# Kernel tuning notes

Hardware: AMD Instinct MI355X
Metric: run time of the kernel (lower is better)

## Reference

```python
import jax, jax.numpy as jnp
import numpy as np

EPS = 1e-5
NH = 4          # num_heads
DH = 128        # head_dim
ALPHA = 1.0 / float(np.sqrt(DH))


def _ln(x, w, b):
    m = x.mean(-1, keepdims=True)
    v = x.var(-1, keepdims=True)
    return (x - m) * jax.lax.rsqrt(v + EPS) * w + b


def setup_inputs() -> dict:
    key = jax.random.key(0)
    ks = jax.random.split(key, 8)
    D = 512                 # hidden_size
    U = 4 * NH * DH         # uvqk linear out = 2048
    B, S, H = 32, 256, 2048  # batch, new tokens/seq, history len/seq
    NT = B * S              # 8192 flattened jagged tokens
    layer_input = jax.random.normal(ks[0], (NT, D), dtype=jnp.float32)
    hist_k = jax.random.normal(ks[1], (B, H, NH, DH), dtype=jnp.float32) * 0.1
    hist_v = jax.random.normal(ks[2], (B, H, NH, DH), dtype=jnp.float32) * 0.1
    # torch init: uniform(-0.5, 0.5); scaled down for numerical sanity
    W_uvqk = (jax.random.uniform(ks[3], (D, U), dtype=jnp.float32) - 0.5) * 0.1
    b_uvqk = (jax.random.uniform(ks[4], (U,), dtype=jnp.float32) - 0.5) * 0.1
    ln_in_w = jnp.ones((D,), jnp.float32)
    ln_in_b = jnp.zeros((D,), jnp.float32)
    ln_out_w = jnp.ones((NH * DH,), jnp.float32)
    ln_out_b = jnp.zeros((NH * DH,), jnp.float32)
    W_proj = jax.random.normal(ks[5], (NH * DH, D), dtype=jnp.float32) * 0.05
    return {
        "layer_input": layer_input, "hist_k": hist_k, "hist_v": hist_v,
        "ln_in_w": ln_in_w, "ln_in_b": ln_in_b,
        "W_uvqk": W_uvqk, "b_uvqk": b_uvqk,
        "ln_out_w": ln_out_w, "ln_out_b": ln_out_b, "W_proj": W_proj,
    }


def reference(layer_input, hist_k, hist_v, ln_in_w, ln_in_b,
              W_uvqk, b_uvqk, ln_out_w, ln_out_b, W_proj):
    B, H, nh, dh = hist_k.shape
    NT, D = layer_input.shape
    S = NT // B
    dspl = nh * dh
    # ln -> linear+bias -> silu (fused u,v,q,k projection)
    x = _ln(layer_input, ln_in_w, ln_in_b)
    uvqk = jax.nn.silu(x @ W_uvqk + b_uvqk)
    u, v, q, k = jnp.split(uvqk, 4, axis=-1)   # order: user, value, query, key
    q = q.reshape(B, S, nh, dh)
    k = k.reshape(B, S, nh, dh)
    v = v.reshape(B, S, nh, dh)
    # paged KV-cache append == concat new k,v after history
    K = jnp.concatenate([hist_k, k], axis=1)   # [B, T, nh, dh], T = H+S
    V = jnp.concatenate([hist_v, v], axis=1)
    T = H + S
    # HSTU varlen attention: silu(alpha * q k^T) with causal delta-q mask,
    # query i sits at global position H+i and may attend to kv pos <= H+i
    scores = jnp.einsum('bsnd,btnd->bnst', q, K) * ALPHA
    mask = jnp.arange(T)[None, :] <= (H + jnp.arange(S))[:, None]  # [S, T]
    p = jnp.where(mask[None, None], jax.nn.silu(scores), 0.0)
    attn = jnp.einsum('bnst,btnd->bsnd', p, V).reshape(NT, dspl)
    # gated output LN, projection, residual
    parallel = u * _ln(attn, ln_out_w, ln_out_b)
    return parallel @ W_proj + layer_input
```

## Files before the change

kernel.cpp:

```cpp
#include <hip/hip_runtime.h>
#include <hip/hip_bf16.h>


typedef __attribute__((ext_vector_type(8))) short v8s;
typedef __attribute__((ext_vector_type(4))) float v4f;
typedef __attribute__((ext_vector_type(16))) float v16f;
typedef __attribute__((ext_vector_type(4))) unsigned short v4us;
typedef __attribute__((ext_vector_type(4))) unsigned int v4u;

#define D_HID 512
#define U_DIM 2048
#define NHEAD 4
#define DHEAD 128
#define BATCH 32
#define SEQ   256
#define HIST  2048
#define NTOK  8192
#define ALPHA_ 0.08838834764831845f
#define EPS_   1e-5f

__device__ __forceinline__ unsigned short f2bf(float f) {
  unsigned int u = __float_as_uint(f);
  u += 0x7FFFu + ((u >> 16) & 1u);
  return (unsigned short)(u >> 16);
}
__device__ __forceinline__ float bf2f(unsigned short s) {
  return __uint_as_float(((unsigned int)s) << 16);
}
__device__ __forceinline__ float siluf(float x) {
  return x * __builtin_amdgcn_rcpf(1.0f + __expf(-x));
}
__device__ __forceinline__ unsigned int cvtpk(float lo, float hi) {
  __hip_bfloat162 h = __float22bfloat162_rn(make_float2(lo, hi));
  union { __hip_bfloat162 h; unsigned int u; } cv; cv.h = h;
  return cv.u;
}

__global__ __launch_bounds__(256) void ln_in_kernel(
    const float* __restrict__ x, const float* __restrict__ w,
    const float* __restrict__ b, unsigned short* __restrict__ out)
{
  int wid = threadIdx.x >> 6, lane = threadIdx.x & 63;
  int row = blockIdx.x * 4 + wid;
  const float* xr = x + (size_t)row * D_HID + lane * 8;
  float4 a0 = *(const float4*)xr;
  float4 a1 = *(const float4*)(xr + 4);
  float v[8] = {a0.x, a0.y, a0.z, a0.w, a1.x, a1.y, a1.z, a1.w};
  float s = 0.f, s2 = 0.f;
#pragma unroll
  for (int j = 0; j < 8; ++j) { s += v[j]; s2 += v[j] * v[j]; }
#pragma unroll
  for (int m = 1; m < 64; m <<= 1) { s += __shfl_xor(s, m, 64); s2 += __shfl_xor(s2, m, 64); }
  float mean = s * (1.f / D_HID);
  float var  = s2 * (1.f / D_HID) - mean * mean;
  float rstd = rsqrtf(var + EPS_);
  const float* wp = w + lane * 8; const float* bp = b + lane * 8;
  float4 w0 = *(const float4*)wp, w1 = *(const float4*)(wp + 4);
  float4 b0 = *(const float4*)bp, b1 = *(const float4*)(bp + 4);
  float wv[8] = {w0.x, w0.y, w0.z, w0.w, w1.x, w1.y, w1.z, w1.w};
  float bv[8] = {b0.x, b0.y, b0.z, b0.w, b1.x, b1.y, b1.z, b1.w};
  v8s o;
#pragma unroll
  for (int j = 0; j < 8; ++j) o[j] = (short)f2bf((v[j] - mean) * rstd * wv[j] + bv[j]);
  *(v8s*)(out + (size_t)row * D_HID + lane * 8) = o;
}

__global__ __launch_bounds__(256) void gated_ln_kernel(
    const float* __restrict__ attn0, const float* __restrict__ attn1,
    const unsigned short* __restrict__ uvqk,
    const float* __restrict__ w, const float* __restrict__ b,
    unsigned short* __restrict__ par)
{
  int wid = threadIdx.x >> 6, lane = threadIdx.x & 63;
  int row = blockIdx.x * 4 + wid;
  size_t off = (size_t)row * D_HID + lane * 8;
  float4 x0 = *(const float4*)(attn0 + off), x1 = *(const float4*)(attn0 + off + 4);
  float4 y0 = *(const float4*)(attn1 + off), y1 = *(const float4*)(attn1 + off + 4);
  float v[8] = {x0.x + y0.x, x0.y + y0.y, x0.z + y0.z, x0.w + y0.w,
                x1.x + y1.x, x1.y + y1.y, x1.z + y1.z, x1.w + y1.w};
  float s = 0.f, s2 = 0.f;
#pragma unroll
  for (int j = 0; j < 8; ++j) { s += v[j]; s2 += v[j] * v[j]; }
#pragma unroll
  for (int m = 1; m < 64; m <<= 1) { s += __shfl_xor(s, m, 64); s2 += __shfl_xor(s2, m, 64); }
  float mean = s * (1.f / D_HID);
  float var  = s2 * (1.f / D_HID) - mean * mean;
  float rstd = rsqrtf(var + EPS_);
  const float* wp = w + lane * 8; const float* bp = b + lane * 8;
  float4 w0 = *(const float4*)wp, w1 = *(const float4*)(wp + 4);
  float4 b0 = *(const float4*)bp, b1 = *(const float4*)(bp + 4);
  float wv[8] = {w0.x, w0.y, w0.z, w0.w, w1.x, w1.y, w1.z, w1.w};
  float bv[8] = {b0.x, b0.y, b0.z, b0.w, b1.x, b1.y, b1.z, b1.w};
  v8s uv = *(const v8s*)(uvqk + (size_t)row * U_DIM + lane * 8);
  v8s o;
#pragma unroll
  for (int j = 0; j < 8; ++j) {
    float u = bf2f((unsigned short)uv[j]);
    o[j] = (short)f2bf(u * ((v[j] - mean) * rstd * wv[j] + bv[j]));
  }
  *(v8s*)(par + (size_t)row * D_HID + lane * 8) = o;
}

__global__ __launch_bounds__(256) void transpose_w_kernel(
    const float* __restrict__ in, unsigned short* __restrict__ out, int R, int C)
{
  __shared__ float tile[32][33];
  int c0 = blockIdx.x * 32, r0 = blockIdx.y * 32;
  int tr = threadIdx.x >> 3;
  int tc = (threadIdx.x & 7) * 4;
  float4 vv = *(const float4*)(in + (size_t)(r0 + tr) * C + c0 + tc);
  tile[tr][tc + 0] = vv.x; tile[tr][tc + 1] = vv.y;
  tile[tr][tc + 2] = vv.z; tile[tr][tc + 3] = vv.w;
  __syncthreads();
  v4us o;
#pragma unroll
  for (int j = 0; j < 4; ++j) o[j] = f2bf(tile[tc + j][tr]);
  *(v4us*)(out + (size_t)(c0 + tr) * R + r0 + tc) = o;
}

template <int EPI>
__global__ __launch_bounds__(256) void gemm_kernel(
    const unsigned short* __restrict__ A, const unsigned short* __restrict__ Bt,
    int K, int N,
    const float* __restrict__ bias, const float* __restrict__ resid,
    unsigned short* __restrict__ outb, float* __restrict__ outf)
{
  __shared__ unsigned short Al[128 * 40];
  __shared__ unsigned short Bl[128 * 40];
  int m0 = blockIdx.x * 128, n0 = blockIdx.y * 128;
  int tid = threadIdx.x, lane = tid & 63, wid = tid >> 6;
  int wr = wid >> 1, wc = wid & 1;
  int lr = lane & 15, lg = lane >> 4;

  v4f acc[4][4];
#pragma unroll
  for (int i = 0; i < 4; ++i)
#pragma unroll
    for (int j = 0; j < 4; ++j) acc[i][j] = (v4f){0.f, 0.f, 0.f, 0.f};

  int srow = tid >> 1;
  int sc   = (tid & 1) * 16;
  const unsigned short* ga = A  + (size_t)(m0 + srow) * K + sc;
  const unsigned short* gb = Bt + (size_t)(n0 + srow) * K + sc;

  for (int k0 = 0; k0 < K; k0 += 32) {
    v8s a0 = *(const v8s*)(ga + k0);
    v8s a1 = *(const v8s*)(ga + k0 + 8);
    v8s b0 = *(const v8s*)(gb + k0);
    v8s b1 = *(const v8s*)(gb + k0 + 8);
    *(v8s*)&Al[srow * 40 + sc]     = a0;
    *(v8s*)&Al[srow * 40 + sc + 8] = a1;
    *(v8s*)&Bl[srow * 40 + sc]     = b0;
    *(v8s*)&Bl[srow * 40 + sc + 8] = b1;
    __syncthreads();
    v8s af[4], bf[4];
#pragma unroll
    for (int mt = 0; mt < 4; ++mt) af[mt] = *(const v8s*)&Al[(wr * 64 + mt * 16 + lr) * 40 + lg * 8];
#pragma unroll
    for (int nt = 0; nt < 4; ++nt) bf[nt] = *(const v8s*)&Bl[(wc * 64 + nt * 16 + lr) * 40 + lg * 8];
#pragma unroll
    for (int mt = 0; mt < 4; ++mt)
#pragma unroll
      for (int nt = 0; nt < 4; ++nt)
        acc[mt][nt] = __builtin_amdgcn_mfma_f32_16x16x32_bf16(af[mt], bf[nt], acc[mt][nt], 0, 0, 0);
    __syncthreads();
  }

#pragma unroll
  for (int nt = 0; nt < 4; ++nt) {
    int col = n0 + wc * 64 + nt * 16 + lr;
    float bi = 0.f;
    if constexpr (EPI == 0) bi = bias[col];
#pragma unroll
    for (int mt = 0; mt < 4; ++mt) {
      int row0 = m0 + wr * 64 + mt * 16 + lg * 4;
#pragma unroll
      for (int r = 0; r < 4; ++r) {
        float xv = acc[mt][nt][r];
        if constexpr (EPI == 0) {
          float rv = siluf(xv + bi);
          if ((unsigned)(col - 2 * D_HID) < (unsigned)D_HID) rv *= ALPHA_;
          outb[(size_t)(row0 + r) * N + col] = f2bf(rv);
        } else {
          outf[(size_t)(row0 + r) * N + col] = xv + resid[(size_t)(row0 + r) * N + col];
        }
      }
    }
  }
}

__global__ __launch_bounds__(512, 2) void attn_kernel(
    const float* __restrict__ histK, const float* __restrict__ histV,
    const unsigned short* __restrict__ uvqk, float* __restrict__ attn_out)
{
  __shared__ __align__(16) unsigned short Kl[2 * 64 * 128];
  __shared__ __align__(16) unsigned short Vt[2 * 128 * 64];

  int bid = blockIdx.x;
  int q   = bid >> 7;
  int b   = (bid >> 2) & 31;
  int n   = bid & 3;
  int tbase0 = q * 1152;
  const int NT = 18;

  int tid = threadIdx.x, lane = tid & 63, w = tid >> 6;
  int l5 = lane & 31;
  int hi = lane >> 5;
  int hi8 = hi * 8;
  int sq = w * 32 + l5;

  v8s qf[8];
  {
    const unsigned short* qp = uvqk + (size_t)(b * SEQ + sq) * U_DIM
                               + 2 * D_HID + n * DHEAD + hi8;
#pragma unroll
    for (int ks = 0; ks < 8; ++ks) qf[ks] = *(const v8s*)(qp + ks * 16);
  }

  v16f oacc[4];
#pragma unroll
  for (int i = 0; i < 4; ++i)
#pragma unroll
    for (int r = 0; r < 16; ++r) oacc[i][r] = 0.f;

  int m     = tid & 15;
  int std0  = m * 8;
  int strow = tid >> 4;

  const float* kbase = histK + (((size_t)b * HIST) * NHEAD + n) * DHEAD + std0;
  const float* vbase = histV + (((size_t)b * HIST) * NHEAD + n) * DHEAD + std0;
  const unsigned short* nkbase = uvqk + (size_t)(b * SEQ) * U_DIM + 3 * D_HID + n * DHEAD + std0;
  const unsigned short* nvbase = uvqk + (size_t)(b * SEQ) * U_DIM + 1 * D_HID + n * DHEAD + std0;

  float4 hx[2][4];
  v8s    nx[2][2];
  int isnew_r = 0;

  auto stage_load = [&](int kt) {
    int tb = tbase0 + kt * 64;
    if (tb < HIST) {
      isnew_r = 0;
#pragma unroll
      for (int p = 0; p < 2; ++p) {
        unsigned off = ((unsigned)(tb + 2 * strow + p)) << 9;
        hx[p][0] = *(const float4*)(kbase + off);
        hx[p][1] = *(const float4*)(kbase + off + 4);
        hx[p][2] = *(const float4*)(vbase + off);
        hx[p][3] = *(const float4*)(vbase + off + 4);
      }
    } else {
      isnew_r = 1;
#pragma unroll
      for (int p = 0; p < 2; ++p) {
        unsigned off = ((unsigned)(tb - HIST + 2 * strow + p)) << 11;
        nx[p][0] = *(const v8s*)(nkbase + off);
        nx[p][1] = *(const v8s*)(nvbase + off);
      }
    }
  };

  auto stage_store = [&](int buf) {
    unsigned short* Kb = &Kl[buf * 8192];
    unsigned short* Vb = &Vt[buf * 8192];
    int t0 = 2 * strow;
    if (!isnew_r) {
#pragma unroll
      for (int p = 0; p < 2; ++p) {
        int t = t0 + p;
        v4u kp;
        kp[0] = cvtpk(hx[p][0].x, hx[p][0].y);
        kp[1] = cvtpk(hx[p][0].z, hx[p][0].w);
        kp[2] = cvtpk(hx[p][1].x, hx[p][1].y);
        kp[3] = cvtpk(hx[p][1].z, hx[p][1].w);
        *(v4u*)&Kb[t * 128 + (std0 ^ ((t & 7) << 3))] = kp;
      }
      float v0[8] = {hx[0][2].x, hx[0][2].y, hx[0][2].z, hx[0][2].w,
                     hx[0][3].x, hx[0][3].y, hx[0][3].z, hx[0][3].w};
      float v1[8] = {hx[1][2].x, hx[1][2].y, hx[1][2].z, hx[1][2].w,
                     hx[1][3].x, hx[1][3].y, hx[1][3].z, hx[1][3].w};
#pragma unroll
      for (int j = 0; j < 8; ++j) {
        int d = std0 + j;
        int col = t0 ^ ((((d >> 3) ^ d) & 7) << 3);
        *(unsigned int*)&Vb[d * 64 + col] = cvtpk(v0[j], v1[j]);
      }
    } else {
#pragma unroll
      for (int p = 0; p < 2; ++p) {
        int t = t0 + p;
        *(v8s*)&Kb[t * 128 + (std0 ^ ((t & 7) << 3))] = nx[p][0];
      }
#pragma unroll
      for (int j = 0; j < 8; ++j) {
        int d = std0 + j;
        int col = t0 ^ ((((d >> 3) ^ d) & 7) << 3);
        unsigned int pk = (unsigned int)(unsigned short)nx[0][1][j]
                        | ((unsigned int)(unsigned short)nx[1][1][j] << 16);
        *(unsigned int*)&Vb[d * 64 + col] = pk;
      }
    }
  };

  stage_load(0);
  stage_store(0);
  stage_load(1);
  __syncthreads();

  for (int kt = 0; kt < NT; ++kt) {
    int cur = kt & 1;
    if (kt + 1 < NT) stage_store(cur ^ 1);
    if (kt + 2 < NT) stage_load(kt + 2);

    int tb = tbase0 + kt * 64;
    bool masked = (tb >= HIST);
    const unsigned short* Kb = &Kl[cur * 8192];
    const unsigned short* Vb = &Vt[cur * 8192];

    __builtin_amdgcn_s_setprio(1);

    v8s pb[4];
#pragma unroll
    for (int tt = 0; tt < 2; ++tt) {
      v16f sa;
#pragma unroll
      for (int r = 0; r < 16; ++r) sa[r] = 0.f;
      int trow = tt * 32 + l5;
      int kx = (trow & 7) << 3;
      int krow = trow * 128;
#pragma unroll
      for (int ks = 0; ks < 8; ++ks) {
        v8s kf = *(const v8s*)&Kb[krow + ((ks * 16 + hi8) ^ kx)];
        sa = __builtin_amdgcn_mfma_f32_32x32x16_bf16(kf, qf[ks], sa, 0, 0, 0);
      }
      unsigned e[8];
      if (masked) {
        int thr = sq - (tb - HIST) - tt * 32 - 4 * hi;
#pragma unroll
        for (int i = 0; i < 8; ++i) {
          int r0 = 2 * i, r1 = 2 * i + 1;
          int tl0 = (r0 & 3) + 8 * (r0 >> 2);
          int tl1 = (r1 & 3) + 8 * (r1 >> 2);
          float p0 = (tl0 <= thr) ? siluf(sa[r0]) : 0.f;
          float p1 = (tl1 <= thr) ? siluf(sa[r1]) : 0.f;
          e[i] = cvtpk(p0, p1);
        }
      } else {
#pragma unroll
        for (int i = 0; i < 8; ++i) e[i] = cvtpk(siluf(sa[2 * i]), siluf(sa[2 * i + 1]));
      }
#pragma unroll
      for (int h = 0; h < 2; ++h) {
        unsigned a0 = e[h * 4 + 0], a1 = e[h * 4 + 1];
        unsigned b0 = e[h * 4 + 2], b1 = e[h * 4 + 3];
        unsigned sa0 = (unsigned)__shfl_xor((int)a0, 32, 64);
        unsigned sa1 = (unsigned)__shfl_xor((int)a1, 32, 64);
        unsigned sb0 = (unsigned)__shfl_xor((int)b0, 32, 64);
        unsigned sb1 = (unsigned)__shfl_xor((int)b1, 32, 64);
        union { unsigned u[4]; v8s s; } U;
        U.u[0] = hi ? sb0 : a0;
        U.u[1] = hi ? sb1 : a1;
        U.u[2] = hi ? b0 : sa0;
        U.u[3] = hi ? b1 : sa1;
        pb[tt * 2 + h] = U.s;
      }
    }

#pragma unroll
    for (int ks = 0; ks < 4; ++ks) {
#pragma unroll
      for (int dt4 = 0; dt4 < 4; ++dt4) {
        int d = dt4 * 32 + l5;
        int col = (ks * 16 + hi8) ^ ((((d >> 3) ^ d) & 7) << 3);
        v8s vf = *(const v8s*)&Vb[d * 64 + col];
        oacc[dt4] = __builtin_amdgcn_mfma_f32_32x32x16_bf16(vf, pb[ks], oacc[dt4], 0, 0, 0);
      }
    }
    __builtin_amdgcn_s_setprio(0);

    if (kt + 1 < NT) __syncthreads();
  }

  {
    float* op = attn_out + (size_t)q * ((size_t)NTOK * D_HID)
              + (size_t)(b * SEQ + sq) * D_HID + n * DHEAD + 4 * hi;
#pragma unroll
    for (int dt4 = 0; dt4 < 4; ++dt4) {
#pragma unroll
      for (int g = 0; g < 4; ++g) {
        float4 o4 = make_float4(oacc[dt4][4 * g + 0], oacc[dt4][4 * g + 1],
                                oacc[dt4][4 * g + 2], oacc[dt4][4 * g + 3]);
        *(float4*)(op + dt4 * 32 + 8 * g) = o4;
      }
    }
  }
}

extern "C" void kernel_launch(void* const* d_in, const int* in_sizes, int n_in,
                              void* d_out, int out_size, void* d_ws, size_t ws_size,
                              hipStream_t stream)
{
  (void)in_sizes; (void)n_in; (void)out_size; (void)ws_size;

  const float* layer_input = (const float*)d_in[0];
  const float* hist_k   = (const float*)d_in[1];
  const float* hist_v   = (const float*)d_in[2];
  const float* ln_in_w  = (const float*)d_in[3];
  const float* ln_in_b  = (const float*)d_in[4];
  const float* W_uvqk   = (const float*)d_in[5];
  const float* b_uvqk   = (const float*)d_in[6];
  const float* ln_out_w = (const float*)d_in[7];
  const float* ln_out_b = (const float*)d_in[8];
  const float* W_proj   = (const float*)d_in[9];
  float* out = (float*)d_out;

  char* ws = (char*)d_ws;
  unsigned short* uvqk    = (unsigned short*)(ws);
  float*          attn0   = (float*)         (ws + (32u << 20));
  float*          attn1   = (float*)         (ws + (48u << 20));
  unsigned short* x_bf    = (unsigned short*)(ws + (48u << 20));
  unsigned short* par     = (unsigned short*)(ws + (64u << 20));
  unsigned short* wt_uvqk = (unsigned short*)(ws + (72u << 20));
  unsigned short* wt_proj = (unsigned short*)(ws + (74u << 20));

  ln_in_kernel<<<dim3(2048), dim3(256), 0, stream>>>(layer_input, ln_in_w, ln_in_b, x_bf);
  transpose_w_kernel<<<dim3(64, 16), dim3(256), 0, stream>>>(W_uvqk, wt_uvqk, 512, 2048);
  transpose_w_kernel<<<dim3(16, 16), dim3(256), 0, stream>>>(W_proj, wt_proj, 512, 512);
  gemm_kernel<0><<<dim3(64, 16), dim3(256), 0, stream>>>(x_bf, wt_uvqk, 512, 2048,
                                                         b_uvqk, nullptr, uvqk, nullptr);
  attn_kernel<<<dim3(256), dim3(512), 0, stream>>>(hist_k, hist_v, uvqk, attn0);
  gated_ln_kernel<<<dim3(2048), dim3(256), 0, stream>>>(attn0, attn1, uvqk, ln_out_w, ln_out_b, par);
  gemm_kernel<1><<<dim3(64, 4), dim3(256), 0, stream>>>(par, wt_proj, 512, 512,
                                                        nullptr, layer_input, nullptr, out);
}
```

Before: 170.3 us.

## Split attention KV into four chunks with 256-thread blocks handling two query sets

```diff
diff --git a/kernel.cpp b/kernel.cpp
--- a/kernel.cpp
+++ b/kernel.cpp
@@ -67,6 +67,7 @@
 
 __global__ __launch_bounds__(256) void gated_ln_kernel(
     const float* __restrict__ attn0, const float* __restrict__ attn1,
+    const float* __restrict__ attn2, const float* __restrict__ attn3,
     const unsigned short* __restrict__ uvqk,
     const float* __restrict__ w, const float* __restrict__ b,
     unsigned short* __restrict__ par)
@@ -76,8 +77,12 @@
   size_t off = (size_t)row * D_HID + lane * 8;
   float4 x0 = *(const float4*)(attn0 + off), x1 = *(const float4*)(attn0 + off + 4);
   float4 y0 = *(const float4*)(attn1 + off), y1 = *(const float4*)(attn1 + off + 4);
-  float v[8] = {x0.x + y0.x, x0.y + y0.y, x0.z + y0.z, x0.w + y0.w,
-                x1.x + y1.x, x1.y + y1.y, x1.z + y1.z, x1.w + y1.w};
+  float4 z0 = *(const float4*)(attn2 + off), z1 = *(const float4*)(attn2 + off + 4);
+  float4 u0 = *(const float4*)(attn3 + off), u1 = *(const float4*)(attn3 + off + 4);
+  float v[8] = {x0.x + y0.x + z0.x + u0.x, x0.y + y0.y + z0.y + u0.y,
+                x0.z + y0.z + z0.z + u0.z, x0.w + y0.w + z0.w + u0.w,
+                x1.x + y1.x + z1.x + u1.x, x1.y + y1.y + z1.y + u1.y,
+                x1.z + y1.z + z1.z + u1.z, x1.w + y1.w + z1.w + u1.w};
   float s = 0.f, s2 = 0.f;
 #pragma unroll
   for (int j = 0; j < 8; ++j) { s += v[j]; s2 += v[j] * v[j]; }
@@ -189,7 +194,7 @@
   }
 }
 
-__global__ __launch_bounds__(512, 2) void attn_kernel(
+__global__ __launch_bounds__(256, 2) void attn_kernel(
     const float* __restrict__ histK, const float* __restrict__ histV,
     const unsigned short* __restrict__ uvqk, float* __restrict__ attn_out)
 {
@@ -200,49 +205,50 @@
   int q   = bid >> 7;
   int b   = (bid >> 2) & 31;
   int n   = bid & 3;
-  int tbase0 = q * 1152;
-  const int NT = 18;
+  int tbase0 = q * 576;
+  const int NT = 9;
 
   int tid = threadIdx.x, lane = tid & 63, w = tid >> 6;
   int l5 = lane & 31;
   int hi = lane >> 5;
   int hi8 = hi * 8;
-  int sq = w * 32 + l5;
-
-  v8s qf[8];
-  {
-    const unsigned short* qp = uvqk + (size_t)(b * SEQ + sq) * U_DIM
+
+  v8s qf[2][8];
+#pragma unroll
+  for (int set = 0; set < 2; ++set) {
+    const unsigned short* qp = uvqk + (size_t)(b * SEQ + w * 64 + set * 32 + l5) * U_DIM
                                + 2 * D_HID + n * DHEAD + hi8;
 #pragma unroll
-    for (int ks = 0; ks < 8; ++ks) qf[ks] = *(const v8s*)(qp + ks * 16);
-  }
-
-  v16f oacc[4];
-#pragma unroll
-  for (int i = 0; i < 4; ++i)
-#pragma unroll
-    for (int r = 0; r < 16; ++r) oacc[i][r] = 0.f;
+    for (int ks = 0; ks < 8; ++ks) qf[set][ks] = *(const v8s*)(qp + ks * 16);
+  }
+
+  v16f oacc[2][4];
+#pragma unroll
+  for (int set = 0; set < 2; ++set)
+#pragma unroll
+    for (int i = 0; i < 4; ++i)
+#pragma unroll
+      for (int r = 0; r < 16; ++r) oacc[set][i][r] = 0.f;
 
   int m     = tid & 15;
   int std0  = m * 8;
   int strow = tid >> 4;
 
-  const float* kbase = histK + (((size_t)b * HIST) * NHEAD + n) * DHEAD + std0;
-  const float* vbase = histV + (((size_t)b * HIST) * NHEAD + n) * DHEAD + std0;
-  const unsigned short* nkbase = uvqk + (size_t)(b * SEQ) * U_DIM + 3 * D_HID + n * DHEAD + std0;
-  const unsigned short* nvbase = uvqk + (size_t)(b * SEQ) * U_DIM + 1 * D_HID + n * DHEAD + std0;
+  const float* kbase = histK + (((size_t)b * HIST) * NHEAD + n) * DHEAD;
+  const float* vbase = histV + (((size_t)b * HIST) * NHEAD + n) * DHEAD;
+  const unsigned short* nkbase = uvqk + (size_t)(b * SEQ) * U_DIM + 3 * D_HID + n * DHEAD;
+  const unsigned short* nvbase = uvqk + (size_t)(b * SEQ) * U_DIM + 1 * D_HID + n * DHEAD;
 
   float4 hx[2][4];
-  v8s    nx[2][2];
   int isnew_r = 0;
 
-  auto stage_load = [&](int kt) {
-    int tb = tbase0 + kt * 64;
+  auto stage_load = [&](int kt, int h) {
+    int tb = tbase0 + kt * 64 + h * 32;
     if (tb < HIST) {
       isnew_r = 0;
 #pragma unroll
       for (int p = 0; p < 2; ++p) {
-        unsigned off = ((unsigned)(tb + 2 * strow + p)) << 9;
+        unsigned off = (((unsigned)(tb + 2 * strow + p)) << 9) + std0;
         hx[p][0] = *(const float4*)(kbase + off);
         hx[p][1] = *(const float4*)(kbase + off + 4);
         hx[p][2] = *(const float4*)(vbase + off);
@@ -252,17 +258,17 @@
       isnew_r = 1;
 #pragma unroll
       for (int p = 0; p < 2; ++p) {
-        unsigned off = ((unsigned)(tb - HIST + 2 * strow + p)) << 11;
-        nx[p][0] = *(const v8s*)(nkbase + off);
-        nx[p][1] = *(const v8s*)(nvbase + off);
+        unsigned off = (((unsigned)(tb - HIST + 2 * strow + p)) << 11) + std0;
+        hx[p][0] = *(const float4*)(nkbase + off);
+        hx[p][2] = *(const float4*)(nvbase + off);
       }
     }
   };
 
-  auto stage_store = [&](int buf) {
+  auto stage_store = [&](int buf, int h) {
     unsigned short* Kb = &Kl[buf * 8192];
     unsigned short* Vb = &Vt[buf * 8192];
-    int t0 = 2 * strow;
+    int t0 = h * 32 + 2 * strow;
     if (!isnew_r) {
 #pragma unroll
       for (int p = 0; p < 2; ++p) {
@@ -285,31 +291,33 @@
         *(unsigned int*)&Vb[d * 64 + col] = cvtpk(v0[j], v1[j]);
       }
     } else {
+      union { float4 f; v8s s; } ck0, ck1, cv0, cv1;
+      ck0.f = hx[0][0]; ck1.f = hx[1][0];
+      cv0.f = hx[0][2]; cv1.f = hx[1][2];
 #pragma unroll
       for (int p = 0; p < 2; ++p) {
         int t = t0 + p;
-        *(v8s*)&Kb[t * 128 + (std0 ^ ((t & 7) << 3))] = nx[p][0];
+        *(v8s*)&Kb[t * 128 + (std0 ^ ((t & 7) << 3))] = p ? ck1.s : ck0.s;
       }
 #pragma unroll
       for (int j = 0; j < 8; ++j) {
         int d = std0 + j;
         int col = t0 ^ ((((d >> 3) ^ d) & 7) << 3);
-        unsigned int pk = (unsigned int)(unsigned short)nx[0][1][j]
-                        | ((unsigned int)(unsigned short)nx[1][1][j] << 16);
+        unsigned int pk = (unsigned int)(unsigned short)cv0.s[j]
+                        | ((unsigned int)(unsigned short)cv1.s[j] << 16);
         *(unsigned int*)&Vb[d * 64 + col] = pk;
       }
     }
   };
 
-  stage_load(0);
-  stage_store(0);
-  stage_load(1);
+  stage_load(0, 0); stage_store(0, 0);
+  stage_load(0, 1); stage_store(0, 1);
+  stage_load(1, 0);
   __syncthreads();
 
   for (int kt = 0; kt < NT; ++kt) {
     int cur = kt & 1;
-    if (kt + 1 < NT) stage_store(cur ^ 1);
-    if (kt + 2 < NT) stage_load(kt + 2);
+    if (kt + 1 < NT) { stage_store(cur ^ 1, 0); stage_load(kt + 1, 1); }
 
     int tb = tbase0 + kt * 64;
     bool masked = (tb >= HIST);
@@ -317,54 +325,63 @@
     const unsigned short* Vb = &Vt[cur * 8192];
 
     __builtin_amdgcn_s_setprio(1);
-
-    v8s pb[4];
+    v8s pb[2][4];
 #pragma unroll
     for (int tt = 0; tt < 2; ++tt) {
-      v16f sa;
-#pragma unroll
-      for (int r = 0; r < 16; ++r) sa[r] = 0.f;
       int trow = tt * 32 + l5;
       int kx = (trow & 7) << 3;
-      int krow = trow * 128;
+      const unsigned short* kr = Kb + trow * 128;
+      v16f sacc[2];
+#pragma unroll
+      for (int r = 0; r < 16; ++r) { sacc[0][r] = 0.f; sacc[1][r] = 0.f; }
 #pragma unroll
       for (int ks = 0; ks < 8; ++ks) {
-        v8s kf = *(const v8s*)&Kb[krow + ((ks * 16 + hi8) ^ kx)];
-        sa = __builtin_amdgcn_mfma_f32_32x32x16_bf16(kf, qf[ks], sa, 0, 0, 0);
-      }
-      unsigned e[8];
-      if (masked) {
-        int thr = sq - (tb - HIST) - tt * 32 - 4 * hi;
-#pragma unroll
-        for (int i = 0; i < 8; ++i) {
-          int r0 = 2 * i, r1 = 2 * i + 1;
-          int tl0 = (r0 & 3) + 8 * (r0 >> 2);
-          int tl1 = (r1 & 3) + 8 * (r1 >> 2);
-          float p0 = (tl0 <= thr) ? siluf(sa[r0]) : 0.f;
-          float p1 = (tl1 <= thr) ? siluf(sa[r1]) : 0.f;
-          e[i] = cvtpk(p0, p1);
+        v8s kf = *(const v8s*)&kr[(ks * 16 + hi8) ^ kx];
+        sacc[0] = __builtin_amdgcn_mfma_f32_32x32x16_bf16(kf, qf[0][ks], sacc[0], 0, 0, 0);
+        sacc[1] = __builtin_amdgcn_mfma_f32_32x32x16_bf16(kf, qf[1][ks], sacc[1], 0, 0, 0);
+      }
+#pragma unroll
+      for (int set = 0; set < 2; ++set) {
+        unsigned e[8];
+        if (masked) {
+          int thr = (w * 64 + set * 32 + l5) - (tb - HIST) - tt * 32 - 4 * hi;
+#pragma unroll
+          for (int i = 0; i < 8; ++i) {
+            int r0 = 2 * i, r1 = r0 + 1;
+            int tl0 = (r0 & 3) + 8 * (r0 >> 2);
+            int tl1 = (r1 & 3) + 8 * (r1 >> 2);
+            float p0 = (tl0 <= thr) ? siluf(sacc[set][r0]) : 0.f;
+            float p1 = (tl1 <= thr) ? siluf(sacc[set][r1]) : 0.f;
+            e[i] = cvtpk(p0, p1);
+          }
+        } else {
+#pragma unroll
+          for (int i = 0; i < 8; ++i)
+            e[i] = cvtpk(siluf(sacc[set][2 * i]), siluf(sacc[set][2 * i + 1]));
         }
-      } else {
-#pragma unroll
-        for (int i = 0; i < 8; ++i) e[i] = cvtpk(siluf(sa[2 * i]), siluf(sa[2 * i + 1]));
-      }
-#pragma unroll
-      for (int h = 0; h < 2; ++h) {
-        unsigned a0 = e[h * 4 + 0], a1 = e[h * 4 + 1];
-        unsigned b0 = e[h * 4 + 2], b1 = e[h * 4 + 3];
-        unsigned sa0 = (unsigned)__shfl_xor((int)a0, 32, 64);
-        unsigned sa1 = (unsigned)__shfl_xor((int)a1, 32, 64);
-        unsigned sb0 = (unsigned)__shfl_xor((int)b0, 32, 64);
-        unsigned sb1 = (unsigned)__shfl_xor((int)b1, 32, 64);
-        union { unsigned u[4]; v8s s; } U;
-        U.u[0] = hi ? sb0 : a0;
-        U.u[1] = hi ? sb1 : a1;
-        U.u[2] = hi ? b0 : sa0;
-        U.u[3] = hi ? b1 : sa1;
-        pb[tt * 2 + h] = U.s;
-      }
-    }
-
+#pragma unroll
+        for (int h = 0; h < 2; ++h) {
+          unsigned a0 = e[h * 4 + 0], a1 = e[h * 4 + 1];
+          unsigned b0 = e[h * 4 + 2], b1 = e[h * 4 + 3];
+          unsigned x0 = (unsigned)__shfl_xor((int)a0, 32, 64);
+          unsigned x1 = (unsigned)__shfl_xor((int)a1, 32, 64);
+          unsigned x2 = (unsigned)__shfl_xor((int)b0, 32, 64);
+          unsigned x3 = (unsigned)__shfl_xor((int)b1, 32, 64);
+          union { unsigned u[4]; v8s s; } U;
+          U.u[0] = hi ? x2 : a0;
+          U.u[1] = hi ? x3 : a1;
+          U.u[2] = hi ? b0 : x0;
+          U.u[3] = hi ? b1 : x1;
+          pb[set][tt * 2 + h] = U.s;
+        }
+      }
+    }
+    __builtin_amdgcn_s_setprio(0);
+
+    if (kt + 1 < NT) stage_store(cur ^ 1, 1);
+    if (kt + 2 < NT) stage_load(kt + 2, 0);
+
+    __builtin_amdgcn_s_setprio(1);
 #pragma unroll
     for (int ks = 0; ks < 4; ++ks) {
 #pragma unroll
@@ -372,7 +389,8 @@
         int d = dt4 * 32 + l5;
         int col = (ks * 16 + hi8) ^ ((((d >> 3) ^ d) & 7) << 3);
         v8s vf = *(const v8s*)&Vb[d * 64 + col];
-        oacc[dt4] = __builtin_amdgcn_mfma_f32_32x32x16_bf16(vf, pb[ks], oacc[dt4], 0, 0, 0);
+        oacc[0][dt4] = __builtin_amdgcn_mfma_f32_32x32x16_bf16(vf, pb[0][ks], oacc[0][dt4], 0, 0, 0);
+        oacc[1][dt4] = __builtin_amdgcn_mfma_f32_32x32x16_bf16(vf, pb[1][ks], oacc[1][dt4], 0, 0, 0);
       }
     }
     __builtin_amdgcn_s_setprio(0);
@@ -380,15 +398,17 @@
     if (kt + 1 < NT) __syncthreads();
   }
 
-  {
+#pragma unroll
+  for (int set = 0; set < 2; ++set) {
     float* op = attn_out + (size_t)q * ((size_t)NTOK * D_HID)
-              + (size_t)(b * SEQ + sq) * D_HID + n * DHEAD + 4 * hi;
+              + (size_t)(b * SEQ + w * 64 + set * 32 + l5) * D_HID
+              + n * DHEAD + 4 * hi;
 #pragma unroll
     for (int dt4 = 0; dt4 < 4; ++dt4) {
 #pragma unroll
       for (int g = 0; g < 4; ++g) {
-        float4 o4 = make_float4(oacc[dt4][4 * g + 0], oacc[dt4][4 * g + 1],
-                                oacc[dt4][4 * g + 2], oacc[dt4][4 * g + 3]);
+        float4 o4 = make_float4(oacc[set][dt4][4 * g + 0], oacc[set][dt4][4 * g + 1],
+                                oacc[set][dt4][4 * g + 2], oacc[set][dt4][4 * g + 3]);
         *(float4*)(op + dt4 * 32 + 8 * g) = o4;
       }
     }
@@ -415,20 +435,23 @@
 
   char* ws = (char*)d_ws;
   unsigned short* uvqk    = (unsigned short*)(ws);
-  float*          attn0   = (float*)         (ws + (32u << 20));
-  float*          attn1   = (float*)         (ws + (48u << 20));
-  unsigned short* x_bf    = (unsigned short*)(ws + (48u << 20));
-  unsigned short* par     = (unsigned short*)(ws + (64u << 20));
-  unsigned short* wt_uvqk = (unsigned short*)(ws + (72u << 20));
-  unsigned short* wt_proj = (unsigned short*)(ws + (74u << 20));
+  float*          attn0   = (float*)         (ws + (32u  << 20));
+  float*          attn1   = (float*)         (ws + (48u  << 20));
+  float*          attn2   = (float*)         (ws + (64u  << 20));
+  float*          attn3   = (float*)         (ws + (80u  << 20));
+  unsigned short* x_bf    = (unsigned short*)(ws + (96u  << 20));
+  unsigned short* par     = (unsigned short*)(ws + (96u  << 20));
+  unsigned short* wt_uvqk = (unsigned short*)(ws + (104u << 20));
+  unsigned short* wt_proj = (unsigned short*)(ws + (106u << 20));
 
   ln_in_kernel<<<dim3(2048), dim3(256), 0, stream>>>(layer_input, ln_in_w, ln_in_b, x_bf);
   transpose_w_kernel<<<dim3(64, 16), dim3(256), 0, stream>>>(W_uvqk, wt_uvqk, 512, 2048);
   transpose_w_kernel<<<dim3(16, 16), dim3(256), 0, stream>>>(W_proj, wt_proj, 512, 512);
   gemm_kernel<0><<<dim3(64, 16), dim3(256), 0, stream>>>(x_bf, wt_uvqk, 512, 2048,
                                                          b_uvqk, nullptr, uvqk, nullptr);
-  attn_kernel<<<dim3(256), dim3(512), 0, stream>>>(hist_k, hist_v, uvqk, attn0);
-  gated_ln_kernel<<<dim3(2048), dim3(256), 0, stream>>>(attn0, attn1, uvqk, ln_out_w, ln_out_b, par);
+  attn_kernel<<<dim3(512), dim3(256), 0, stream>>>(hist_k, hist_v, uvqk, attn0);
+  gated_ln_kernel<<<dim3(2048), dim3(256), 0, stream>>>(attn0, attn1, attn2, attn3,
+                                                        uvqk, ln_out_w, ln_out_b, par);
   gemm_kernel<1><<<dim3(64, 4), dim3(256), 0, stream>>>(par, wt_proj, 512, 512,
                                                         nullptr, layer_input, nullptr, out);
 }
```

After: 387.0 us. +127.2%, slower.

## Split attention blocks by query half and exchange P tiles across waves via LDS

Applied to the files above, without the earlier changes.

```diff
diff --git a/kernel.cpp b/kernel.cpp
--- a/kernel.cpp
+++ b/kernel.cpp
@@ -189,25 +189,32 @@
   }
 }
 
-__global__ __launch_bounds__(512, 2) void attn_kernel(
+__global__ __launch_bounds__(512, 4) void attn_kernel(
     const float* __restrict__ histK, const float* __restrict__ histV,
     const unsigned short* __restrict__ uvqk, float* __restrict__ attn_out)
 {
   __shared__ __align__(16) unsigned short Kl[2 * 64 * 128];
   __shared__ __align__(16) unsigned short Vt[2 * 128 * 64];
+  __shared__ unsigned int Pex[8][8][64];
 
   int bid = blockIdx.x;
-  int q   = bid >> 7;
+  int th  = bid >> 8;
+  int qb  = (bid >> 7) & 1;
   int b   = (bid >> 2) & 31;
   int n   = bid & 3;
-  int tbase0 = q * 1152;
-  const int NT = 18;
+  int tbase0 = th * 1152;
+  int NT = 18;
+  {
+    int nt2 = (HIST + qb * 128 + 127 - tbase0) / 64 + 1;
+    if (nt2 < NT) NT = nt2;
+  }
 
   int tid = threadIdx.x, lane = tid & 63, w = tid >> 6;
+  int g  = w & 3;
+  int h  = w >> 2;
   int l5 = lane & 31;
-  int hi = lane >> 5;
-  int hi8 = hi * 8;
-  int sq = w * 32 + l5;
+  int hi = lane >> 5, hi8 = hi * 8;
+  int sq = qb * 128 + g * 32 + l5;
 
   v8s qf[8];
   {
@@ -217,9 +224,9 @@
     for (int ks = 0; ks < 8; ++ks) qf[ks] = *(const v8s*)(qp + ks * 16);
   }
 
-  v16f oacc[4];
-#pragma unroll
-  for (int i = 0; i < 4; ++i)
+  v16f oacc[2];
+#pragma unroll
+  for (int i = 0; i < 2; ++i)
 #pragma unroll
     for (int r = 0; r < 16; ++r) oacc[i][r] = 0.f;
 
@@ -233,7 +240,6 @@
   const unsigned short* nvbase = uvqk + (size_t)(b * SEQ) * U_DIM + 1 * D_HID + n * DHEAD + std0;
 
   float4 hx[2][4];
-  v8s    nx[2][2];
   int isnew_r = 0;
 
   auto stage_load = [&](int kt) {
@@ -253,8 +259,8 @@
 #pragma unroll
       for (int p = 0; p < 2; ++p) {
         unsigned off = ((unsigned)(tb - HIST + 2 * strow + p)) << 11;
-        nx[p][0] = *(const v8s*)(nkbase + off);
-        nx[p][1] = *(const v8s*)(nvbase + off);
+        hx[p][0] = *(const float4*)(const void*)(nkbase + off);
+        hx[p][2] = *(const float4*)(const void*)(nvbase + off);
       }
     }
   };
@@ -285,17 +291,20 @@
         *(unsigned int*)&Vb[d * 64 + col] = cvtpk(v0[j], v1[j]);
       }
     } else {
+      union { float4 f; v8s s; } ck0, ck1, cv0, cv1;
+      ck0.f = hx[0][0]; ck1.f = hx[1][0];
+      cv0.f = hx[0][2]; cv1.f = hx[1][2];
 #pragma unroll
       for (int p = 0; p < 2; ++p) {
         int t = t0 + p;
-        *(v8s*)&Kb[t * 128 + (std0 ^ ((t & 7) << 3))] = nx[p][0];
+        *(v8s*)&Kb[t * 128 + (std0 ^ ((t & 7) << 3))] = p ? ck1.s : ck0.s;
       }
 #pragma unroll
       for (int j = 0; j < 8; ++j) {
         int d = std0 + j;
         int col = t0 ^ ((((d >> 3) ^ d) & 7) << 3);
-        unsigned int pk = (unsigned int)(unsigned short)nx[0][1][j]
-                        | ((unsigned int)(unsigned short)nx[1][1][j] << 16);
+        unsigned int pk = (unsigned int)(unsigned short)cv0.s[j]
+                        | ((unsigned int)(unsigned short)cv1.s[j] << 16);
         *(unsigned int*)&Vb[d * 64 + col] = pk;
       }
     }
@@ -316,15 +325,14 @@
     const unsigned short* Kb = &Kl[cur * 8192];
     const unsigned short* Vb = &Vt[cur * 8192];
 
+    v8s pb[4];
+
     __builtin_amdgcn_s_setprio(1);
-
-    v8s pb[4];
-#pragma unroll
-    for (int tt = 0; tt < 2; ++tt) {
+    {
       v16f sa;
 #pragma unroll
       for (int r = 0; r < 16; ++r) sa[r] = 0.f;
-      int trow = tt * 32 + l5;
+      int trow = h * 32 + l5;
       int kx = (trow & 7) << 3;
       int krow = trow * 128;
 #pragma unroll
@@ -334,7 +342,7 @@
       }
       unsigned e[8];
       if (masked) {
-        int thr = sq - (tb - HIST) - tt * 32 - 4 * hi;
+        int thr = sq - (tb - HIST) - h * 32 - 4 * hi;
 #pragma unroll
         for (int i = 0; i < 8; ++i) {
           int r0 = 2 * i, r1 = 2 * i + 1;
@@ -349,9 +357,9 @@
         for (int i = 0; i < 8; ++i) e[i] = cvtpk(siluf(sa[2 * i]), siluf(sa[2 * i + 1]));
       }
 #pragma unroll
-      for (int h = 0; h < 2; ++h) {
-        unsigned a0 = e[h * 4 + 0], a1 = e[h * 4 + 1];
-        unsigned b0 = e[h * 4 + 2], b1 = e[h * 4 + 3];
+      for (int hh = 0; hh < 2; ++hh) {
+        unsigned a0 = e[hh * 4 + 0], a1 = e[hh * 4 + 1];
+        unsigned b0 = e[hh * 4 + 2], b1 = e[hh * 4 + 3];
         unsigned sa0 = (unsigned)__shfl_xor((int)a0, 32, 64);
         unsigned sa1 = (unsigned)__shfl_xor((int)a1, 32, 64);
         unsigned sb0 = (unsigned)__shfl_xor((int)b0, 32, 64);
@@ -361,15 +369,39 @@
         U.u[1] = hi ? sb1 : a1;
         U.u[2] = hi ? b0 : sa0;
         U.u[3] = hi ? b1 : sa1;
-        pb[tt * 2 + h] = U.s;
-      }
-    }
-
+        pb[2 * h + hh] = U.s;
+      }
+    }
+    __builtin_amdgcn_s_setprio(0);
+
+    {
+      union { v8s s; unsigned u[4]; } F0, F1;
+      F0.s = pb[2 * h]; F1.s = pb[2 * h + 1];
+#pragma unroll
+      for (int j = 0; j < 4; ++j) {
+        Pex[w][j][lane]     = F0.u[j];
+        Pex[w][j + 4][lane] = F1.u[j];
+      }
+    }
+    __syncthreads();
+    {
+      int hp = 1 - h;
+      union { unsigned u[4]; v8s s; } G0, G1;
+#pragma unroll
+      for (int j = 0; j < 4; ++j) {
+        G0.u[j] = Pex[w ^ 4][j][lane];
+        G1.u[j] = Pex[w ^ 4][j + 4][lane];
+      }
+      pb[2 * hp]     = G0.s;
+      pb[2 * hp + 1] = G1.s;
+    }
+
+    __builtin_amdgcn_s_setprio(1);
 #pragma unroll
     for (int ks = 0; ks < 4; ++ks) {
 #pragma unroll
-      for (int dt4 = 0; dt4 < 4; ++dt4) {
-        int d = dt4 * 32 + l5;
+      for (int dt4 = 0; dt4 < 2; ++dt4) {
+        int d = h * 64 + dt4 * 32 + l5;
         int col = (ks * 16 + hi8) ^ ((((d >> 3) ^ d) & 7) << 3);
         v8s vf = *(const v8s*)&Vb[d * 64 + col];
         oacc[dt4] = __builtin_amdgcn_mfma_f32_32x32x16_bf16(vf, pb[ks], oacc[dt4], 0, 0, 0);
@@ -381,15 +413,15 @@
   }
 
   {
-    float* op = attn_out + (size_t)q * ((size_t)NTOK * D_HID)
-              + (size_t)(b * SEQ + sq) * D_HID + n * DHEAD + 4 * hi;
-#pragma unroll
-    for (int dt4 = 0; dt4 < 4; ++dt4) {
-#pragma unroll
-      for (int g = 0; g < 4; ++g) {
-        float4 o4 = make_float4(oacc[dt4][4 * g + 0], oacc[dt4][4 * g + 1],
-                                oacc[dt4][4 * g + 2], oacc[dt4][4 * g + 3]);
-        *(float4*)(op + dt4 * 32 + 8 * g) = o4;
+    float* op = attn_out + (size_t)th * ((size_t)NTOK * D_HID)
+              + (size_t)(b * SEQ + sq) * D_HID + n * DHEAD + h * 64 + 4 * hi;
+#pragma unroll
+    for (int dt4 = 0; dt4 < 2; ++dt4) {
+#pragma unroll
+      for (int gq = 0; gq < 4; ++gq) {
+        float4 o4 = make_float4(oacc[dt4][4 * gq + 0], oacc[dt4][4 * gq + 1],
+                                oacc[dt4][4 * gq + 2], oacc[dt4][4 * gq + 3]);
+        *(float4*)(op + dt4 * 32 + 8 * gq) = o4;
       }
     }
   }
@@ -427,7 +459,7 @@
   transpose_w_kernel<<<dim3(16, 16), dim3(256), 0, stream>>>(W_proj, wt_proj, 512, 512);
   gemm_kernel<0><<<dim3(64, 16), dim3(256), 0, stream>>>(x_bf, wt_uvqk, 512, 2048,
                                                          b_uvqk, nullptr, uvqk, nullptr);
-  attn_kernel<<<dim3(256), dim3(512), 0, stream>>>(hist_k, hist_v, uvqk, attn0);
+  attn_kernel<<<dim3(512), dim3(512), 0, stream>>>(hist_k, hist_v, uvqk, attn0);
   gated_ln_kernel<<<dim3(2048), dim3(256), 0, stream>>>(attn0, attn1, uvqk, ln_out_w, ln_out_b, par);
   gemm_kernel<1><<<dim3(64, 4), dim3(256), 0, stream>>>(par, wt_proj, 512, 512,
                                                         nullptr, layer_input, nullptr, out);
```

New measurement: 511.9 us. 3.01x slower.

## Use direct global-to-LDS loads with swizzle in GEMM and interleave QK MFMA chains

Applied to the files above, without the earlier changes.

```diff
diff --git a/kernel.cpp b/kernel.cpp
--- a/kernel.cpp
+++ b/kernel.cpp
@@ -125,12 +125,13 @@
     const float* __restrict__ bias, const float* __restrict__ resid,
     unsigned short* __restrict__ outb, float* __restrict__ outf)
 {
-  __shared__ unsigned short Al[128 * 40];
-  __shared__ unsigned short Bl[128 * 40];
+  __shared__ unsigned short Al[128 * 64];
+  __shared__ unsigned short Bl[128 * 64];
   int m0 = blockIdx.x * 128, n0 = blockIdx.y * 128;
   int tid = threadIdx.x, lane = tid & 63, wid = tid >> 6;
   int wr = wid >> 1, wc = wid & 1;
   int lr = lane & 15, lg = lane >> 4;
+  int rkey = (lr & 7) << 3;
 
   v4f acc[4][4];
 #pragma unroll
@@ -138,31 +139,38 @@
 #pragma unroll
     for (int j = 0; j < 4; ++j) acc[i][j] = (v4f){0.f, 0.f, 0.f, 0.f};
 
-  int srow = tid >> 1;
-  int sc   = (tid & 1) * 16;
-  const unsigned short* ga = A  + (size_t)(m0 + srow) * K + sc;
-  const unsigned short* gb = Bt + (size_t)(n0 + srow) * K + sc;
-
-  for (int k0 = 0; k0 < K; k0 += 32) {
-    v8s a0 = *(const v8s*)(ga + k0);
-    v8s a1 = *(const v8s*)(ga + k0 + 8);
-    v8s b0 = *(const v8s*)(gb + k0);
-    v8s b1 = *(const v8s*)(gb + k0 + 8);
-    *(v8s*)&Al[srow * 40 + sc]     = a0;
-    *(v8s*)&Al[srow * 40 + sc + 8] = a1;
-    *(v8s*)&Bl[srow * 40 + sc]     = b0;
-    *(v8s*)&Bl[srow * 40 + sc + 8] = b1;
+  int srow = tid >> 3;
+  int scol = ((tid & 7) * 8) ^ ((srow & 7) << 3);
+  const unsigned short* gA = A  + (size_t)(m0 + srow) * K + scol;
+  const unsigned short* gB = Bt + (size_t)(n0 + srow) * K + scol;
+
+  for (int k0 = 0; k0 < K; k0 += 64) {
+#pragma unroll
+    for (int c = 0; c < 4; ++c) {
+      __builtin_amdgcn_global_load_lds(
+          (const __attribute__((address_space(1))) unsigned int*)(gA + (size_t)(c * 32) * K + k0),
+          (__attribute__((address_space(3))) unsigned int*)&Al[c * 2048 + wid * 512], 16, 0, 0);
+      __builtin_amdgcn_global_load_lds(
+          (const __attribute__((address_space(1))) unsigned int*)(gB + (size_t)(c * 32) * K + k0),
+          (__attribute__((address_space(3))) unsigned int*)&Bl[c * 2048 + wid * 512], 16, 0, 0);
+    }
+    asm volatile("s_waitcnt vmcnt(0)" ::: "memory");
     __syncthreads();
-    v8s af[4], bf[4];
-#pragma unroll
-    for (int mt = 0; mt < 4; ++mt) af[mt] = *(const v8s*)&Al[(wr * 64 + mt * 16 + lr) * 40 + lg * 8];
-#pragma unroll
-    for (int nt = 0; nt < 4; ++nt) bf[nt] = *(const v8s*)&Bl[(wc * 64 + nt * 16 + lr) * 40 + lg * 8];
-#pragma unroll
-    for (int mt = 0; mt < 4; ++mt)
+#pragma unroll
+    for (int kk = 0; kk < 2; ++kk) {
+      v8s af[4], bf[4];
+#pragma unroll
+      for (int mt = 0; mt < 4; ++mt)
+        af[mt] = *(const v8s*)&Al[(wr * 64 + mt * 16 + lr) * 64 + ((kk * 32 + lg * 8) ^ rkey)];
 #pragma unroll
       for (int nt = 0; nt < 4; ++nt)
-        acc[mt][nt] = __builtin_amdgcn_mfma_f32_16x16x32_bf16(af[mt], bf[nt], acc[mt][nt], 0, 0, 0);
+        bf[nt] = *(const v8s*)&Bl[(wc * 64 + nt * 16 + lr) * 64 + ((kk * 32 + lg * 8) ^ rkey)];
+#pragma unroll
+      for (int mt = 0; mt < 4; ++mt)
+#pragma unroll
+        for (int nt = 0; nt < 4; ++nt)
+          acc[mt][nt] = __builtin_amdgcn_mfma_f32_16x16x32_bf16(af[mt], bf[nt], acc[mt][nt], 0, 0, 0);
+    }
     __syncthreads();
   }
 
@@ -319,49 +327,54 @@
     __builtin_amdgcn_s_setprio(1);
 
     v8s pb[4];
-#pragma unroll
-    for (int tt = 0; tt < 2; ++tt) {
-      v16f sa;
-#pragma unroll
-      for (int r = 0; r < 16; ++r) sa[r] = 0.f;
-      int trow = tt * 32 + l5;
-      int kx = (trow & 7) << 3;
-      int krow = trow * 128;
+    {
+      v16f sa0, sa1;
+#pragma unroll
+      for (int r = 0; r < 16; ++r) { sa0[r] = 0.f; sa1[r] = 0.f; }
+      int kx = (l5 & 7) << 3;
+      int krow = l5 * 128;
 #pragma unroll
       for (int ks = 0; ks < 8; ++ks) {
-        v8s kf = *(const v8s*)&Kb[krow + ((ks * 16 + hi8) ^ kx)];
-        sa = __builtin_amdgcn_mfma_f32_32x32x16_bf16(kf, qf[ks], sa, 0, 0, 0);
-      }
-      unsigned e[8];
-      if (masked) {
-        int thr = sq - (tb - HIST) - tt * 32 - 4 * hi;
-#pragma unroll
-        for (int i = 0; i < 8; ++i) {
-          int r0 = 2 * i, r1 = 2 * i + 1;
-          int tl0 = (r0 & 3) + 8 * (r0 >> 2);
-          int tl1 = (r1 & 3) + 8 * (r1 >> 2);
-          float p0 = (tl0 <= thr) ? siluf(sa[r0]) : 0.f;
-          float p1 = (tl1 <= thr) ? siluf(sa[r1]) : 0.f;
-          e[i] = cvtpk(p0, p1);
+        int off = (ks * 16 + hi8) ^ kx;
+        v8s kf0 = *(const v8s*)&Kb[krow + off];
+        v8s kf1 = *(const v8s*)&Kb[krow + 4096 + off];
+        sa0 = __builtin_amdgcn_mfma_f32_32x32x16_bf16(kf0, qf[ks], sa0, 0, 0, 0);
+        sa1 = __builtin_amdgcn_mfma_f32_32x32x16_bf16(kf1, qf[ks], sa1, 0, 0, 0);
+      }
+#pragma unroll
+      for (int tt = 0; tt < 2; ++tt) {
+        v16f sa = tt ? sa1 : sa0;
+        unsigned e[8];
+        if (masked) {
+          int thr = sq - (tb - HIST) - tt * 32 - 4 * hi;
+#pragma unroll
+          for (int i = 0; i < 8; ++i) {
+            int r0 = 2 * i, r1 = 2 * i + 1;
+            int tl0 = (r0 & 3) + 8 * (r0 >> 2);
+            int tl1 = (r1 & 3) + 8 * (r1 >> 2);
+            float p0 = (tl0 <= thr) ? siluf(sa[r0]) : 0.f;
+            float p1 = (tl1 <= thr) ? siluf(sa[r1]) : 0.f;
+            e[i] = cvtpk(p0, p1);
+          }
+        } else {
+#pragma unroll
+          for (int i = 0; i < 8; ++i) e[i] = cvtpk(siluf(sa[2 * i]), siluf(sa[2 * i + 1]));
         }
-      } else {
-#pragma unroll
-        for (int i = 0; i < 8; ++i) e[i] = cvtpk(siluf(sa[2 * i]), siluf(sa[2 * i + 1]));
-      }
-#pragma unroll
-      for (int h = 0; h < 2; ++h) {
-        unsigned a0 = e[h * 4 + 0], a1 = e[h * 4 + 1];
-        unsigned b0 = e[h * 4 + 2], b1 = e[h * 4 + 3];
-        unsigned sa0 = (unsigned)__shfl_xor((int)a0, 32, 64);
-        unsigned sa1 = (unsigned)__shfl_xor((int)a1, 32, 64);
-        unsigned sb0 = (unsigned)__shfl_xor((int)b0, 32, 64);
-        unsigned sb1 = (unsigned)__shfl_xor((int)b1, 32, 64);
-        union { unsigned u[4]; v8s s; } U;
-        U.u[0] = hi ? sb0 : a0;
-        U.u[1] = hi ? sb1 : a1;
-        U.u[2] = hi ? b0 : sa0;
-        U.u[3] = hi ? b1 : sa1;
-        pb[tt * 2 + h] = U.s;
+#pragma unroll
+        for (int h = 0; h < 2; ++h) {
+          unsigned a0 = e[h * 4 + 0], a1 = e[h * 4 + 1];
+          unsigned b0 = e[h * 4 + 2], b1 = e[h * 4 + 3];
+          unsigned sa0u = (unsigned)__shfl_xor((int)a0, 32, 64);
+          unsigned sa1u = (unsigned)__shfl_xor((int)a1, 32, 64);
+          unsigned sb0u = (unsigned)__shfl_xor((int)b0, 32, 64);
+          unsigned sb1u = (unsigned)__shfl_xor((int)b1, 32, 64);
+          union { unsigned u[4]; v8s s; } U;
+          U.u[0] = hi ? sb0u : a0;
+          U.u[1] = hi ? sb1u : a1;
+          U.u[2] = hi ? b0 : sa0u;
+          U.u[3] = hi ? b1 : sa1u;
+          pb[tt * 2 + h] = U.s;
+        }
       }
     }
 
```

New measurement: 157.5 us, median of 2. 1.08x faster.
